# Kernel optimization log

Hardware: AMD Instinct MI355X
Metric: run time of the kernel (lower is better)

## Reference

```python
import jax, jax.numpy as jnp
import numpy as np

N = 8192       # number of nodes
T = 4          # number of edge types
E = 131072     # edges per type
D = 32         # edge_emb_dim
H = 4          # num_head_attentions
NEG_SLOPE = 0.2


def setup_inputs() -> dict:
    key = jax.random.key(0)
    k1, k2, k3, k4 = jax.random.split(key, 4)
    scores = jax.random.normal(k1, (N, 1), dtype=jnp.float32)
    edge_type_emb = jax.random.normal(k2, (T, D), dtype=jnp.float32)
    edge_index = jax.random.randint(k3, (T, 2, E), 0, N, dtype=jnp.int32)
    # xavier-normal-ish init for the per-head attention weights [H, D+2, 1]
    std = float(np.sqrt(2.0 / (D + 2 + 1)))
    attention_weight = jax.random.normal(k4, (H, D + 2, 1), dtype=jnp.float32) * std
    return {"scores": scores, "edge_type_emb": edge_type_emb,
            "edge_index": edge_index, "attention_weight": attention_weight}


def _head_forward(W_h, scores, edge_type_emb, src, tgt):
    # W_h: [D+2, 1]; split the concat-matmul: cat([s_src, emb, s_tgt]) @ W
    w = W_h[:, 0]
    w_src, w_emb, w_tgt = w[0], w[1:D + 1], w[D + 1]
    s = scores[:, 0]                               # [N]
    # per-edge attention logits, vectorized over edge types: [T, E]
    emb_term = edge_type_emb @ w_emb               # [T]
    vals = s[src] * w_src + s[tgt] * w_tgt + emb_term[:, None]
    # scatter-add into dense NxN (duplicates accumulate, matching += semantics)
    A = jnp.zeros((N, N), dtype=scores.dtype).at[src.ravel(), tgt.ravel()].add(vals.ravel())
    A = jnp.where(A >= 0, A, NEG_SLOPE * A)        # LeakyReLU(0.2)
    A = jax.nn.softmax(A, axis=-1)                 # dense row softmax
    return A @ scores                               # [N, 1]


def reference(scores, edge_type_emb, edge_index, attention_weight):
    src = edge_index[:, 0, :]  # [T, E]
    tgt = edge_index[:, 1, :]
    head_fn = lambda W_h: _head_forward(W_h, scores, edge_type_emb, src, tgt)
    outs = jax.vmap(head_fn)(attention_weight)      # [H, N, 1]
    return jnp.mean(outs, axis=0)                   # [N, 1]
```

## Files before the change

kernel.cpp:

```cpp
#include <hip/hip_runtime.h>
#include <stdint.h>


#define NN 8192
#define TT 4
#define EE 131072
#define DD 32
#define HH 4
#define NEG_SLOPE 0.2f

#define NB  256
#define RPB 32
#define CAP 2560
#define SEG 128
#define EMPTY 0xFFFFFFFFu


__global__ void k0(const float* __restrict__ scores,
                   const float* __restrict__ ete,
                   const float* __restrict__ aw,
                   uint32_t* __restrict__ cursor,
                   float* __restrict__ f) {
    int tid = threadIdx.x;
    if (tid < NB) cursor[tid] = 0;
    __shared__ float red[256];
    float s = 0.f;
    for (int i = tid; i < NN; i += 256) s += scores[i];
    red[tid] = s;
    __syncthreads();
    for (int off = 128; off > 0; off >>= 1) {
        if (tid < off) red[tid] += red[tid + off];
        __syncthreads();
    }
    if (tid == 0) f[0] = red[0];
    if (tid < HH) {
        f[1 + tid] = aw[tid * (DD + 2)];
        f[5 + tid] = aw[tid * (DD + 2) + DD + 1];
    }
    if (tid < HH * TT) {
        int h = tid / TT, t = tid % TT;
        float acc = 0.f;
        for (int d = 0; d < DD; ++d)
            acc += ete[t * DD + d] * aw[h * (DD + 2) + 1 + d];
        f[9 + tid] = acc;
    }
}

#define A_EPT 16
__global__ void __launch_bounds__(256) kA(const int* __restrict__ ei,
                                          uint32_t* __restrict__ cursor,
                                          uint32_t* __restrict__ buf) {
    __shared__ uint32_t hist[NB];
    __shared__ uint32_t baseh[NB];
    int tid = threadIdx.x;
    if (tid < NB) hist[tid] = 0;
    __syncthreads();

    uint32_t gtid = blockIdx.x * 256u + (uint32_t)tid;
    uint32_t t  = gtid >> 13;
    uint32_t e0 = (gtid & 8191u) * A_EPT;
    const int4* sp = (const int4*)(ei + (size_t)(t * 2) * EE + e0);
    const int4* tp = (const int4*)(ei + (size_t)(t * 2 + 1) * EE + e0);

    uint32_t val[A_EPT];
    uint32_t rnk[A_EPT];
    #pragma unroll
    for (int k = 0; k < A_EPT / 4; ++k) {
        int4 s4 = sp[k];
        int4 t4 = tp[k];
        val[k*4+0] = ((uint32_t)s4.x << 15) | ((uint32_t)t4.x << 2) | t;
        val[k*4+1] = ((uint32_t)s4.y << 15) | ((uint32_t)t4.y << 2) | t;
        val[k*4+2] = ((uint32_t)s4.z << 15) | ((uint32_t)t4.z << 2) | t;
        val[k*4+3] = ((uint32_t)s4.w << 15) | ((uint32_t)t4.w << 2) | t;
    }
    #pragma unroll
    for (int k = 0; k < A_EPT; ++k)
        rnk[k] = atomicAdd(&hist[val[k] >> 20], 1u);
    __syncthreads();
    if (tid < NB) baseh[tid] = atomicAdd(&cursor[tid], hist[tid]);
    __syncthreads();
    #pragma unroll
    for (int k = 0; k < A_EPT; ++k) {
        uint32_t b = val[k] >> 20;
        buf[b * CAP + baseh[b] + rnk[k]] = val[k] & 0xFFFFFu;
    }
}

__global__ void __launch_bounds__(256) kB(const float* __restrict__ scores,
                                          const uint32_t* __restrict__ cursor,
                                          const uint32_t* __restrict__ buf,
                                          const float* __restrict__ f,
                                          float* __restrict__ out) {
    __shared__ uint32_t tab[RPB * SEG];
    int tid = threadIdx.x;
    for (int i = tid; i < RPB * SEG; i += 256) tab[i] = EMPTY;

    float st = f[0];
    float wsrc[HH], wtgt[HH], em[HH * TT];
    #pragma unroll
    for (int h = 0; h < HH; ++h) { wsrc[h] = f[1 + h]; wtgt[h] = f[5 + h]; }
    #pragma unroll
    for (int k = 0; k < HH * TT; ++k) em[k] = f[9 + k];
    __syncthreads();

    uint32_t b = blockIdx.x;
    uint32_t n = cursor[b];
    if (n > CAP) n = CAP;
    const uint32_t* bb = buf + b * CAP;

    for (uint32_t i = tid; i < n; i += 256) {
        uint32_t v   = bb[i];
        uint32_t row = v >> 15;
        uint32_t tgt = (v >> 2) & 8191u;
        uint32_t tt  = v & 3u;
        uint32_t inc = 1u << (13 + 4 * tt);
        uint32_t fresh = tgt | inc;
        uint32_t pos = (tgt * 2654435761u) >> 25;
        uint32_t base = row * SEG;
        while (true) {
            uint32_t cur = atomicCAS(&tab[base + pos], EMPTY, fresh);
            if (cur == EMPTY) break;
            bool done = false;
            while ((cur & 0x1FFFu) == tgt) {
                uint32_t prev = atomicCAS(&tab[base + pos], cur, cur + inc);
                if (prev == cur) { done = true; break; }
                cur = prev;
            }
            if (done) break;
            pos = (pos + 1) & (SEG - 1);
        }
    }
    __syncthreads();

    int wave = tid >> 6, lane = tid & 63;
    #pragma unroll
    for (int rr = 0; rr < 8; ++rr) {
        int r = wave * 8 + rr;
        float si = scores[b * RPB + r];
        float num[HH] = {0.f, 0.f, 0.f, 0.f};
        float den[HH] = {0.f, 0.f, 0.f, 0.f};
        #pragma unroll
        for (int half = 0; half < 2; ++half) {
            uint32_t w = tab[r * SEG + half * 64 + lane];
            if (w != EMPTY) {
                uint32_t tgt = w & 0x1FFFu;
                float c0 = (float)((w >> 13) & 15u);
                float c1 = (float)((w >> 17) & 15u);
                float c2 = (float)((w >> 21) & 15u);
                float c3 = (float)((w >> 25) & 15u);
                float ctot = c0 + c1 + c2 + c3;
                float sj = scores[tgt];
                #pragma unroll
                for (int h = 0; h < HH; ++h) {
                    float a = ctot * (si * wsrc[h] + sj * wtgt[h])
                            + c0 * em[h * 4 + 0] + c1 * em[h * 4 + 1]
                            + c2 * em[h * 4 + 2] + c3 * em[h * 4 + 3];
                    a = (a >= 0.f) ? a : NEG_SLOPE * a;
                    float ex = expf(a) - 1.f;
                    den[h] += ex;
                    num[h] += ex * sj;
                }
            }
        }
        #pragma unroll
        for (int m = 32; m > 0; m >>= 1) {
            #pragma unroll
            for (int h = 0; h < HH; ++h) {
                num[h] += __shfl_xor(num[h], m, 64);
                den[h] += __shfl_xor(den[h], m, 64);
            }
        }
        if (lane == 0) {
            float acc = 0.f;
            #pragma unroll
            for (int h = 0; h < HH; ++h)
                acc += (st + num[h]) / ((float)NN + den[h]);
            out[b * RPB + r] = acc * (1.f / HH);
        }
    }
}

extern "C" void kernel_launch(void* const* d_in, const int* in_sizes, int n_in,
                              void* d_out, int out_size, void* d_ws, size_t ws_size,
                              hipStream_t stream) {
    const float* scores = (const float*)d_in[0];
    const float* ete    = (const float*)d_in[1];
    const int*   ei     = (const int*)d_in[2];
    const float* aw     = (const float*)d_in[3];
    float* out = (float*)d_out;

    uint32_t* cursor = (uint32_t*)d_ws;
    float*    f      = (float*)(cursor + NB);
    uint32_t* buf    = cursor + NB + 64;

    k0<<<1, 256, 0, stream>>>(scores, ete, aw, cursor, f);
    kA<<<128, 256, 0, stream>>>(ei, cursor, buf);
    kB<<<NB, 256, 0, stream>>>(scores, cursor, buf, f, out);
}
```

Baseline: 105.2 us.

## Bucket edges per producer block to drop global cursor atomics and merge setup kernel

Edges are now bucketed into 1024 row buckets (8 rows each) and written into per-(bucket, producer block) slots of fixed capacity, with a byte count array, so no global atomic cursor or cursor reset is needed. The scalar setup kernel is folded into the bucketing kernel as an extra block, removing one launch. The consumer kernel reads each block's run with two threads per run and uses four times as many blocks over fewer rows. The risk is that per-slot capacity of 20 silently drops edges if a producer block hits a bucket more often than that, and the setup block runs concurrently with the same grid.

```diff
diff --git a/kernel.cpp b/kernel.cpp
--- a/kernel.cpp
+++ b/kernel.cpp
@@ -9,51 +9,50 @@
 #define HH 4
 #define NEG_SLOPE 0.2f
 
-#define NB  256
-#define RPB 32
-#define CAP 2560
-#define SEG 128
+#define NB    1024
+#define RPB   8
+#define SEG   128
+#define ABLK  128
+#define CAPBB 20
+#define A_EPT 16
 #define EMPTY 0xFFFFFFFFu
 
 
-__global__ void k0(const float* __restrict__ scores,
-                   const float* __restrict__ ete,
-                   const float* __restrict__ aw,
-                   uint32_t* __restrict__ cursor,
-                   float* __restrict__ f) {
+__global__ void __launch_bounds__(256) kA(const int* __restrict__ ei,
+                                          const float* __restrict__ scores,
+                                          const float* __restrict__ ete,
+                                          const float* __restrict__ aw,
+                                          uint8_t* __restrict__ cnt,
+                                          uint32_t* __restrict__ buf,
+                                          float* __restrict__ f) {
     int tid = threadIdx.x;
-    if (tid < NB) cursor[tid] = 0;
-    __shared__ float red[256];
-    float s = 0.f;
-    for (int i = tid; i < NN; i += 256) s += scores[i];
-    red[tid] = s;
-    __syncthreads();
-    for (int off = 128; off > 0; off >>= 1) {
-        if (tid < off) red[tid] += red[tid + off];
+    if (blockIdx.x == ABLK) {
+        __shared__ float red[256];
+        float s = 0.f;
+        for (int i = tid; i < NN; i += 256) s += scores[i];
+        red[tid] = s;
         __syncthreads();
-    }
-    if (tid == 0) f[0] = red[0];
-    if (tid < HH) {
-        f[1 + tid] = aw[tid * (DD + 2)];
-        f[5 + tid] = aw[tid * (DD + 2) + DD + 1];
-    }
-    if (tid < HH * TT) {
-        int h = tid / TT, t = tid % TT;
-        float acc = 0.f;
-        for (int d = 0; d < DD; ++d)
-            acc += ete[t * DD + d] * aw[h * (DD + 2) + 1 + d];
-        f[9 + tid] = acc;
-    }
-}
-
-#define A_EPT 16
-__global__ void __launch_bounds__(256) kA(const int* __restrict__ ei,
-                                          uint32_t* __restrict__ cursor,
-                                          uint32_t* __restrict__ buf) {
+        for (int off = 128; off > 0; off >>= 1) {
+            if (tid < off) red[tid] += red[tid + off];
+            __syncthreads();
+        }
+        if (tid == 0) f[0] = red[0];
+        if (tid < HH) {
+            f[1 + tid] = aw[tid * (DD + 2)];
+            f[5 + tid] = aw[tid * (DD + 2) + DD + 1];
+        }
+        if (tid < HH * TT) {
+            int h = tid / TT, t = tid % TT;
+            float acc = 0.f;
+            for (int d = 0; d < DD; ++d)
+                acc += ete[t * DD + d] * aw[h * (DD + 2) + 1 + d];
+            f[9 + tid] = acc;
+        }
+        return;
+    }
+
     __shared__ uint32_t hist[NB];
-    __shared__ uint32_t baseh[NB];
-    int tid = threadIdx.x;
-    if (tid < NB) hist[tid] = 0;
+    for (int i = tid; i < NB; i += 256) hist[i] = 0;
     __syncthreads();
 
     uint32_t gtid = blockIdx.x * 256u + (uint32_t)tid;
@@ -75,25 +74,33 @@
     }
     #pragma unroll
     for (int k = 0; k < A_EPT; ++k)
-        rnk[k] = atomicAdd(&hist[val[k] >> 20], 1u);
-    __syncthreads();
-    if (tid < NB) baseh[tid] = atomicAdd(&cursor[tid], hist[tid]);
-    __syncthreads();
+        rnk[k] = atomicAdd(&hist[val[k] >> 18], 1u);
+    __syncthreads();
+
+    for (int i = tid; i < NB; i += 256) {
+        uint32_t c = hist[i];
+        cnt[(uint32_t)i * ABLK + blockIdx.x] = (uint8_t)(c > CAPBB ? CAPBB : c);
+    }
     #pragma unroll
     for (int k = 0; k < A_EPT; ++k) {
-        uint32_t b = val[k] >> 20;
-        buf[b * CAP + baseh[b] + rnk[k]] = val[k] & 0xFFFFFu;
+        if (rnk[k] < CAPBB) {
+            uint32_t b = val[k] >> 18;
+            buf[((size_t)b * ABLK + blockIdx.x) * CAPBB + rnk[k]] = val[k] & 0x3FFFFu;
+        }
     }
 }
 
 __global__ void __launch_bounds__(256) kB(const float* __restrict__ scores,
-                                          const uint32_t* __restrict__ cursor,
+                                          const uint8_t* __restrict__ cnt,
                                           const uint32_t* __restrict__ buf,
                                           const float* __restrict__ f,
                                           float* __restrict__ out) {
     __shared__ uint32_t tab[RPB * SEG];
+    __shared__ uint8_t  cc[ABLK];
     int tid = threadIdx.x;
     for (int i = tid; i < RPB * SEG; i += 256) tab[i] = EMPTY;
+    uint32_t b = blockIdx.x;
+    if (tid < ABLK) cc[tid] = cnt[b * ABLK + tid];
 
     float st = f[0];
     float wsrc[HH], wtgt[HH], em[HH * TT];
@@ -103,13 +110,11 @@
     for (int k = 0; k < HH * TT; ++k) em[k] = f[9 + k];
     __syncthreads();
 
-    uint32_t b = blockIdx.x;
-    uint32_t n = cursor[b];
-    if (n > CAP) n = CAP;
-    const uint32_t* bb = buf + b * CAP;
-
-    for (uint32_t i = tid; i < n; i += 256) {
-        uint32_t v   = bb[i];
+    int run = tid >> 1, sub = tid & 1;
+    const uint32_t* rb = buf + ((size_t)b * ABLK + run) * CAPBB;
+    int c = cc[run];
+    for (int i = sub; i < c; i += 2) {
+        uint32_t v   = rb[i];
         uint32_t row = v >> 15;
         uint32_t tgt = (v >> 2) & 8191u;
         uint32_t tt  = v & 3u;
@@ -134,8 +139,8 @@
 
     int wave = tid >> 6, lane = tid & 63;
     #pragma unroll
-    for (int rr = 0; rr < 8; ++rr) {
-        int r = wave * 8 + rr;
+    for (int rr = 0; rr < 2; ++rr) {
+        int r = wave * 2 + rr;
         float si = scores[b * RPB + r];
         float num[HH] = {0.f, 0.f, 0.f, 0.f};
         float den[HH] = {0.f, 0.f, 0.f, 0.f};
@@ -189,11 +194,10 @@
     const float* aw     = (const float*)d_in[3];
     float* out = (float*)d_out;
 
-    uint32_t* cursor = (uint32_t*)d_ws;
-    float*    f      = (float*)(cursor + NB);
-    uint32_t* buf    = cursor + NB + 64;
-
-    k0<<<1, 256, 0, stream>>>(scores, ete, aw, cursor, f);
-    kA<<<128, 256, 0, stream>>>(ei, cursor, buf);
-    kB<<<NB, 256, 0, stream>>>(scores, cursor, buf, f, out);
+    uint8_t*  cnt = (uint8_t*)d_ws;
+    float*    f   = (float*)((char*)d_ws + NB * ABLK);
+    uint32_t* buf = (uint32_t*)((char*)d_ws + NB * ABLK + 1024);
+
+    kA<<<ABLK + 1, 256, 0, stream>>>(ei, scores, ete, aw, cnt, buf, f);
+    kB<<<NB, 256, 0, stream>>>(scores, cnt, buf, f, out);
 }
```

After: 92.52 us. -12.0%, faster.
